# Performance work log

Measured on AMD Instinct MI355X. Metric: run time of the kernel, lower is better.

Reference implementation:

```python
import jax, jax.numpy as jnp
import numpy as np
from jax import lax

DIM = 2048
N_HEADS = 16
N_KV = 4
HEAD_DIM = DIM // N_HEADS  # 128
ROPE_BASE = 10000.0
SEQ = 4096
BSZ = 1


def bitlinear(x, W):
    # per-row abs-mean scale (detached), ternary round/clamp, straight-through blend
    s = lax.stop_gradient(jnp.clip(jnp.mean(jnp.abs(W), axis=1, keepdims=True), 1e-5, None))
    wt = jnp.clip(jnp.round(W / s), -1.0, 1.0)
    w = lax.stop_gradient(wt - W) + W  # straight-through
    return x @ (w * s).T


def rms_norm(x):
    eps = jnp.finfo(x.dtype).eps
    return x * lax.rsqrt(jnp.mean(x * x, axis=-1, keepdims=True) + eps)


def rope(x, cos, sin):
    half = x.shape[-1] // 2
    x1, x2 = x[..., :half], x[..., half:]
    return jnp.concatenate((x1 * cos + x2 * sin, -x1 * sin + x2 * cos), axis=-1)


def setup_inputs() -> dict:
    key = jax.random.key(0)
    ks = jax.random.split(key, 6)
    kv_dim = N_KV * HEAD_DIM
    return {
        "x": jax.random.normal(ks[0], (BSZ, SEQ, DIM), dtype=jnp.float32),
        "wq": jax.random.normal(ks[1], (DIM, DIM), dtype=jnp.float32) * 0.02,
        "wk": jax.random.normal(ks[2], (kv_dim, DIM), dtype=jnp.float32) * 0.02,
        "wv": jax.random.normal(ks[3], (kv_dim, DIM), dtype=jnp.float32) * 0.02,
        "wp": jax.random.normal(ks[4], (DIM, DIM), dtype=jnp.float32) * 0.02,
        "q_gain": jnp.ones((N_HEADS,), dtype=jnp.float32),
    }


def reference(x, wq, wk, wv, wp, q_gain):
    b, s, d = x.shape
    q = bitlinear(x, wq).reshape(b, s, N_HEADS, HEAD_DIM).transpose(0, 2, 1, 3)  # bhsd
    k = bitlinear(x, wk).reshape(b, s, N_KV, HEAD_DIM).transpose(0, 2, 1, 3)
    v = bitlinear(x, wv).reshape(b, s, N_KV, HEAD_DIM).transpose(0, 2, 1, 3)

    q = rms_norm(q)
    k = rms_norm(k)

    inv_freq = 1.0 / ROPE_BASE ** (jnp.arange(0, HEAD_DIM, 2, dtype=jnp.float32) / HEAD_DIM)
    t = jnp.arange(s, dtype=jnp.float32)
    freqs = jnp.outer(t, inv_freq)  # [s, hd/2]
    cos = jnp.cos(freqs)[None, None].astype(q.dtype)
    sin = jnp.sin(freqs)[None, None].astype(q.dtype)
    q = rope(q, cos, sin)
    k = rope(k, cos, sin)

    q = q * q_gain.astype(q.dtype)[None, :, None, None]

    groups = N_HEADS // N_KV
    k = jnp.repeat(k, groups, axis=1)  # GQA expand to [b, H, s, hd]
    v = jnp.repeat(v, groups, axis=1)

    scale = 1.0 / np.sqrt(HEAD_DIM)
    scores = jnp.einsum("bhqd,bhkd->bhqk", q, k) * scale
    causal = jnp.tril(jnp.ones((s, s), dtype=bool))
    scores = jnp.where(causal[None, None], scores, jnp.finfo(scores.dtype).min)
    attn = jax.nn.softmax(scores, axis=-1)
    y = jnp.einsum("bhqk,bhkd->bhqd", attn, v)

    y = y.transpose(0, 2, 1, 3).reshape(b, s, d)
    return bitlinear(y, wp)
```

## Files before the change

### kernel.cpp

```cpp
#include <hip/hip_runtime.h>
#include <math.h>

typedef unsigned short u16;
typedef short s16x8 __attribute__((ext_vector_type(8)));
typedef float f32x4 __attribute__((ext_vector_type(4)));
typedef u16 u16x4 __attribute__((ext_vector_type(4)));

static constexpr size_t OFF_XB   = 0;
static constexpr size_t OFF_WQKV = 16777216;
static constexpr size_t OFF_WP   = 29360128;
static constexpr size_t OFF_QKV  = 37748736;
static constexpr size_t OFF_KH   = 88080384;
static constexpr size_t OFF_VT   = 92274688;

__device__ __forceinline__ u16 f2bf(float f) {
  union { float f; unsigned u; } v; v.f = f;
  unsigned r = v.u + 0x7fffu + ((v.u >> 16) & 1u);
  return (u16)(r >> 16);
}

__device__ __forceinline__ void async16(const u16* g, u16* lds) {
  __builtin_amdgcn_global_load_lds(
      (const __attribute__((address_space(1))) void*)g,
      (__attribute__((address_space(3))) void*)lds, 16, 0, 0);
}

__global__ __launch_bounds__(256) void quant_rows(const float* __restrict__ W,
                                                  u16* __restrict__ out) {
  const int row = blockIdx.x, tid = threadIdx.x;
  const float* src = W + (size_t)row * 2048 + tid * 8;
  float4 a = *(const float4*)(src);
  float4 b = *(const float4*)(src + 4);
  float asum = fabsf(a.x)+fabsf(a.y)+fabsf(a.z)+fabsf(a.w)
             + fabsf(b.x)+fabsf(b.y)+fabsf(b.z)+fabsf(b.w);
  #pragma unroll
  for (int off = 1; off < 64; off <<= 1) asum += __shfl_xor(asum, off, 64);
  __shared__ float red[4];
  if ((tid & 63) == 0) red[tid >> 6] = asum;
  __syncthreads();
  float s = fmaxf((red[0]+red[1]+red[2]+red[3]) * (1.0f/2048.0f), 1e-5f);
  float v[8] = {a.x,a.y,a.z,a.w,b.x,b.y,b.z,b.w};
  u16* dst = out + (size_t)row * 2048 + tid * 8;
  #pragma unroll
  for (int i = 0; i < 8; i++) {
    float q = rintf(v[i] / s);
    q = fminf(fmaxf(q, -1.f), 1.f);
    dst[i] = f2bf(q * s);
  }
}

__global__ __launch_bounds__(256) void cvt_bf16(const float* __restrict__ in,
                                                u16* __restrict__ out) {
  size_t i = ((size_t)blockIdx.x * 256 + threadIdx.x) * 4;
  float4 v = *(const float4*)(in + i);
  u16x4 o;
  o.x = f2bf(v.x); o.y = f2bf(v.y); o.z = f2bf(v.z); o.w = f2bf(v.w);
  *(u16x4*)(out + i) = o;
}

__global__ __launch_bounds__(256) void gemm_bt(const u16* __restrict__ A,
                                               const u16* __restrict__ B,
                                               float* __restrict__ C,
                                               int M, int N, int K) {
  __shared__ u16 sA[128 * 32];
  __shared__ u16 sB[128 * 32];
  const int tid = threadIdx.x;
  const int lane = tid & 63;
  const int wid = tid >> 6;
  const int lr = lane & 15, lq = lane >> 4;
  const int wm = (wid >> 1) * 64, wn = (wid & 1) * 64;
  const size_t m0 = (size_t)blockIdx.y * 128, n0 = (size_t)blockIdx.x * 128;

  const int r0 = tid >> 2, c0 = (tid & 3) * 8;
  const u16* Ab0 = A + (m0 + r0) * (size_t)K + c0;
  const u16* Ab1 = A + (m0 + 64 + r0) * (size_t)K + c0;
  const u16* Bb0 = B + (n0 + r0) * (size_t)K + c0;
  const u16* Bb1 = B + (n0 + 64 + r0) * (size_t)K + c0;
  u16* sA0 = &sA[tid * 8];
  u16* sA1 = &sA[(256 + tid) * 8];
  u16* sB0 = &sB[tid * 8];
  u16* sB1 = &sB[(256 + tid) * 8];

  f32x4 acc[4][4] = {};

  for (int kt = 0; kt < K; kt += 32) {
    async16(Ab0 + kt, sA0);
    async16(Ab1 + kt, sA1);
    async16(Bb0 + kt, sB0);
    async16(Bb1 + kt, sB1);
    __syncthreads();
    s16x8 af[4], bf[4];
    #pragma unroll
    for (int mt = 0; mt < 4; mt++)
      af[mt] = *(const s16x8*)&sA[(wm + mt * 16 + lr) * 32 + lq * 8];
    #pragma unroll
    for (int nt = 0; nt < 4; nt++)
      bf[nt] = *(const s16x8*)&sB[(wn + nt * 16 + lr) * 32 + lq * 8];
    #pragma unroll
    for (int mt = 0; mt < 4; mt++)
      #pragma unroll
      for (int nt = 0; nt < 4; nt++)
        acc[mt][nt] = __builtin_amdgcn_mfma_f32_16x16x32_bf16(af[mt], bf[nt], acc[mt][nt], 0, 0, 0);
    __syncthreads();
  }
  #pragma unroll
  for (int mt = 0; mt < 4; mt++)
    #pragma unroll
    for (int nt = 0; nt < 4; nt++)
      #pragma unroll
      for (int r = 0; r < 4; r++) {
        size_t m = m0 + wm + mt * 16 + lq * 4 + r;
        size_t n = n0 + wn + nt * 16 + lr;
        C[m * (size_t)N + n] = acc[mt][nt][r];
      }
}

__global__ __launch_bounds__(256) void prep_qk(const float* __restrict__ qkv,
                                               const float* __restrict__ qgain,
                                               u16* __restrict__ Qh,
                                               u16* __restrict__ Kh) {
  const int s = blockIdx.y;
  const int j = blockIdx.x * 4 + (threadIdx.x >> 6);
  const int t = threadIdx.x & 63;
  const float* row = qkv + (size_t)s * 3072 + (size_t)j * 128;
  float x1 = row[t], x2 = row[t + 64];
  float ss = x1 * x1 + x2 * x2;
  #pragma unroll
  for (int off = 1; off < 64; off <<= 1) ss += __shfl_xor(ss, off, 64);
  float rn = rsqrtf(ss * (1.0f / 128.0f) + 1.1920929e-07f);
  float invf = exp2f(-(float)t * 0.20762050593048096f);
  float ang = (float)s * invf;
  float sn, c;
  sincosf(ang, &sn, &c);
  if (j < 16) {
    float g = qgain[j] * 0.12751738f;
    float q1 = x1 * rn, q2 = x2 * rn;
    float o1 = (q1 * c + q2 * sn) * g;
    float o2 = (-q1 * sn + q2 * c) * g;
    u16* dst = Qh + ((size_t)j * 4096 + s) * 128;
    dst[t] = f2bf(o1); dst[t + 64] = f2bf(o2);
  } else {
    float k1 = x1 * rn, k2 = x2 * rn;
    float o1 = k1 * c + k2 * sn;
    float o2 = -k1 * sn + k2 * c;
    u16* dst = Kh + ((size_t)(j - 16) * 4096 + s) * 128;
    dst[t] = f2bf(o1); dst[t + 64] = f2bf(o2);
  }
}

__global__ __launch_bounds__(256) void vtrans(const float* __restrict__ qkv,
                                              u16* __restrict__ Vtg) {
  __shared__ float tile[64][67];
  const int tid = threadIdx.x;
  const int s0 = blockIdx.y * 64;
  const int c0 = blockIdx.x * 64;
  #pragma unroll
  for (int it = 0; it < 4; it++) {
    int i = it * 256 + tid;
    int r = i >> 4, c = (i & 15) * 4;
    float4 v = *(const float4*)(qkv + (size_t)(s0 + r) * 3072 + 2560 + c0 + c);
    tile[r][c] = v.x; tile[r][c + 1] = v.y; tile[r][c + 2] = v.z; tile[r][c + 3] = v.w;
  }
  __syncthreads();
  #pragma unroll
  for (int it = 0; it < 2; it++) {
    int i = it * 256 + tid;
    int dl = i >> 3, sc = (i & 7) * 8;
    s16x8 ov;
    #pragma unroll
    for (int jj = 0; jj < 8; jj++) ov[jj] = (short)f2bf(tile[sc + jj][dl]);
    *(s16x8*)&Vtg[(size_t)(c0 + dl) * 4096 + s0 + sc] = ov;
  }
}

__global__ __launch_bounds__(256) void attn(const u16* __restrict__ Q,
                                            const u16* __restrict__ Kh,
                                            const u16* __restrict__ Vt,
                                            u16* __restrict__ Y) {
  const int h = blockIdx.x & 15;
  const int qt = 63 - (blockIdx.x >> 4);
  const int kvh = h >> 2;
  const int tid = threadIdx.x, lane = tid & 63, wid = tid >> 6;
  const int lr = lane & 15, lq = lane >> 4;

  __shared__ u16 sK[64][136];
  __shared__ u16 sVt[128][72];
  __shared__ u16 sP[4][16][72];

  const int q0 = qt * 64;
  s16x8 qf[4];
  {
    const u16* qp = Q + ((size_t)h * 4096 + q0 + wid * 16 + lr) * 128 + lq * 8;
    #pragma unroll
    for (int kc = 0; kc < 4; kc++) qf[kc] = *(const s16x8*)(qp + kc * 32);
  }
  f32x4 oacc[8] = {};
  float mrow[4], lrow[4];
  #pragma unroll
  for (int r = 0; r < 4; r++) { mrow[r] = -1e30f; lrow[r] = 0.f; }

  const u16* Kbase = Kh + (size_t)kvh * 4096 * 128;
  const u16* Vbase = Vt + (size_t)kvh * 128 * 4096;

  for (int t = 0; t <= qt; ++t) {
    #pragma unroll
    for (int it = 0; it < 4; it++) {
      int idx = it * 256 + tid;
      int kr = idx >> 4, kc = (idx & 15) * 8;
      *(s16x8*)&sK[kr][kc] = *(const s16x8*)(Kbase + ((size_t)(t * 64 + kr)) * 128 + kc);
    }
    #pragma unroll
    for (int it = 0; it < 4; it++) {
      int idx = it * 256 + tid;
      int vd = idx >> 3, vc = (idx & 7) * 8;
      *(s16x8*)&sVt[vd][vc] = *(const s16x8*)(Vbase + (size_t)vd * 4096 + t * 64 + vc);
    }
    __syncthreads();

    f32x4 sacc[4] = {};
    #pragma unroll
    for (int nt = 0; nt < 4; nt++)
      #pragma unroll
      for (int kc = 0; kc < 4; kc++) {
        s16x8 kf = *(const s16x8*)&sK[nt * 16 + lr][kc * 32 + lq * 8];
        sacc[nt] = __builtin_amdgcn_mfma_f32_16x16x32_bf16(qf[kc], kf, sacc[nt], 0, 0, 0);
      }
    if (t == qt) {
      #pragma unroll
      for (int nt = 0; nt < 4; nt++)
        #pragma unroll
        for (int r = 0; r < 4; r++)
          if (nt * 16 + lr > wid * 16 + lq * 4 + r) sacc[nt][r] = -1e30f;
    }
    float mx[4];
    #pragma unroll
    for (int r = 0; r < 4; r++)
      mx[r] = fmaxf(fmaxf(sacc[0][r], sacc[1][r]), fmaxf(sacc[2][r], sacc[3][r]));
    #pragma unroll
    for (int off = 1; off < 16; off <<= 1)
      #pragma unroll
      for (int r = 0; r < 4; r++) mx[r] = fmaxf(mx[r], __shfl_xor(mx[r], off, 64));
    float mnew[4], alpha[4], rsum[4];
    #pragma unroll
    for (int r = 0; r < 4; r++) {
      mnew[r] = fmaxf(mrow[r], mx[r]);
      alpha[r] = exp2f(mrow[r] - mnew[r]);
      rsum[r] = 0.f;
    }
    #pragma unroll
    for (int nt = 0; nt < 4; nt++)
      #pragma unroll
      for (int r = 0; r < 4; r++) {
        float p = exp2f(sacc[nt][r] - mnew[r]);
        rsum[r] += p;
        sP[wid][lq * 4 + r][nt * 16 + lr] = f2bf(p);
      }
    #pragma unroll
    for (int off = 1; off < 16; off <<= 1)
      #pragma unroll
      for (int r = 0; r < 4; r++) rsum[r] += __shfl_xor(rsum[r], off, 64);
    #pragma unroll
    for (int r = 0; r < 4; r++) { lrow[r] = lrow[r] * alpha[r] + rsum[r]; mrow[r] = mnew[r]; }
    #pragma unroll
    for (int dt = 0; dt < 8; dt++)
      #pragma unroll
      for (int r = 0; r < 4; r++) oacc[dt][r] *= alpha[r];
    #pragma unroll
    for (int kc = 0; kc < 2; kc++) {
      s16x8 pf = *(const s16x8*)&sP[wid][lr][kc * 32 + lq * 8];
      #pragma unroll
      for (int dt = 0; dt < 8; dt++) {
        s16x8 vf = *(const s16x8*)&sVt[dt * 16 + lr][kc * 32 + lq * 8];
        oacc[dt] = __builtin_amdgcn_mfma_f32_16x16x32_bf16(pf, vf, oacc[dt], 0, 0, 0);
      }
    }
    __syncthreads();
  }
  float invl[4];
  #pragma unroll
  for (int r = 0; r < 4; r++) invl[r] = 1.0f / lrow[r];
  #pragma unroll
  for (int dt = 0; dt < 8; dt++)
    #pragma unroll
    for (int r = 0; r < 4; r++) {
      int qg = q0 + wid * 16 + lq * 4 + r;
      int d = dt * 16 + lr;
      Y[(size_t)qg * 2048 + h * 128 + d] = f2bf(oacc[dt][r] * invl[r]);
    }
}

extern "C" void kernel_launch(void* const* d_in, const int* in_sizes, int n_in,
                              void* d_out, int out_size, void* d_ws, size_t ws_size,
                              hipStream_t stream) {
  const float* x  = (const float*)d_in[0];
  const float* wq = (const float*)d_in[1];
  const float* wk = (const float*)d_in[2];
  const float* wv = (const float*)d_in[3];
  const float* wp = (const float*)d_in[4];
  const float* qg = (const float*)d_in[5];
  float* out = (float*)d_out;
  char* ws = (char*)d_ws;

  u16*   XB   = (u16*)(ws + OFF_XB);
  u16*   WQKV = (u16*)(ws + OFF_WQKV);
  u16*   WP   = (u16*)(ws + OFF_WP);
  float* QKV  = (float*)(ws + OFF_QKV);
  u16*   QH   = XB;
  u16*   KH   = (u16*)(ws + OFF_KH);
  u16*   VT   = (u16*)(ws + OFF_VT);
  u16*   Yb   = (u16*)(ws + OFF_QKV);

  quant_rows<<<2048, 256, 0, stream>>>(wq, WQKV);
  quant_rows<<<512,  256, 0, stream>>>(wk, WQKV + (size_t)2048 * 2048);
  quant_rows<<<512,  256, 0, stream>>>(wv, WQKV + (size_t)2560 * 2048);
  quant_rows<<<2048, 256, 0, stream>>>(wp, WP);
  cvt_bf16<<<8192, 256, 0, stream>>>(x, XB);
  gemm_bt<<<dim3(24, 32), 256, 0, stream>>>(XB, WQKV, QKV, 4096, 3072, 2048);
  prep_qk<<<dim3(5, 4096), 256, 0, stream>>>(QKV, qg, QH, KH);
  vtrans<<<dim3(8, 64), 256, 0, stream>>>(QKV, VT);
  attn<<<1024, 256, 0, stream>>>(QH, KH, VT, Yb);
  gemm_bt<<<dim3(16, 32), 256, 0, stream>>>(Yb, WP, out, 4096, 2048, 2048);
}
```

Baseline: 467.9 us.

## Use 128-row query tiles with split-KV for long tiles and combine kernel

The attention kernel now processes 128 query rows per block, with each wave handling two 16-row fragments, so every K/V tile loaded into LDS is reused twice as much. Query tiles in the upper half of the sequence are split into two KV chunks whose partial outputs and max/sum statistics go to a workspace, and a new combine kernel merges them. Blocks are ordered longest-first for load balance. Other changes: the row sum is taken from a ones-row appended to V via MFMA, the accumulator rescale is skipped when no row max grows, and the launch bounds request two blocks per CU. The cost is more registers per thread, an extra kernel launch, extra workspace traffic, and bf16 truncation instead of rounding for P.

```diff
diff --git a/kernel.cpp b/kernel.cpp
--- a/kernel.cpp
+++ b/kernel.cpp
@@ -10,6 +10,7 @@
 static constexpr size_t OFF_WQKV = 16777216;
 static constexpr size_t OFF_WP   = 29360128;
 static constexpr size_t OFF_QKV  = 37748736;
+static constexpr size_t OFF_PART = 37748736 + 16777216;
 static constexpr size_t OFF_KH   = 88080384;
 static constexpr size_t OFF_VT   = 92274688;
 
@@ -173,41 +174,62 @@
   }
 }
 
-__global__ __launch_bounds__(256) void attn(const u16* __restrict__ Q,
-                                            const u16* __restrict__ Kh,
-                                            const u16* __restrict__ Vt,
-                                            u16* __restrict__ Y) {
-  const int h = blockIdx.x & 15;
-  const int qt = 63 - (blockIdx.x >> 4);
-  const int kvh = h >> 2;
+__global__ __launch_bounds__(256, 2) void attn(const u16* __restrict__ Q,
+                                               const u16* __restrict__ Kh,
+                                               const u16* __restrict__ Vt,
+                                               u16* __restrict__ Y,
+                                               float* __restrict__ Opart,
+                                               float* __restrict__ MLpart) {
   const int tid = threadIdx.x, lane = tid & 63, wid = tid >> 6;
   const int lr = lane & 15, lq = lane >> 4;
 
+  int rem = blockIdx.x, s = 32;
+  for (;;) {
+    int cnt = (s >= 17 ? 32 : 0) + (((s & 1) == 0) ? 16 : 0);
+    if (rem < cnt) break;
+    rem -= cnt; --s;
+  }
+  int qt, chunk, h, split;
+  if (s >= 17 && rem < 32) { split = 1; qt = s - 1; chunk = rem >> 4; h = rem & 15; }
+  else { split = 0; if (s >= 17) rem -= 32; qt = (s >> 1) - 1; chunk = 0; h = rem & 15; }
+  const int t0 = split ? chunk * (qt + 1) : 0;
+  const int t1 = split ? t0 + qt + 1 : 2 * qt + 2;
+  const int kvh = h >> 2;
+  const int qbase = qt * 128;
+
   __shared__ u16 sK[64][136];
-  __shared__ u16 sVt[128][72];
-  __shared__ u16 sP[4][16][72];
-
-  const int q0 = qt * 64;
-  s16x8 qf[4];
-  {
-    const u16* qp = Q + ((size_t)h * 4096 + q0 + wid * 16 + lr) * 128 + lq * 8;
-    #pragma unroll
-    for (int kc = 0; kc < 4; kc++) qf[kc] = *(const s16x8*)(qp + kc * 32);
-  }
-  f32x4 oacc[8] = {};
-  float mrow[4], lrow[4];
-  #pragma unroll
-  for (int r = 0; r < 4; r++) { mrow[r] = -1e30f; lrow[r] = 0.f; }
+  __shared__ u16 sVt[144][72];
+  __shared__ u16 sP[4][32][72];
+
+  for (int i = tid; i < 16 * 72; i += 256) {
+    int r = i / 72, c = i - r * 72;
+    sVt[128 + r][c] = (r == 0) ? (u16)0x3F80 : (u16)0;
+  }
+
+  s16x8 qf[2][4];
+  #pragma unroll
+  for (int f = 0; f < 2; f++) {
+    const u16* qp = Q + ((size_t)h * 4096 + qbase + wid * 32 + f * 16 + lr) * 128 + lq * 8;
+    #pragma unroll
+    for (int kc = 0; kc < 4; kc++) qf[f][kc] = *(const s16x8*)(qp + kc * 32);
+  }
+
+  f32x4 oacc[2][9] = {};
+  float mrow[2][4];
+  #pragma unroll
+  for (int f = 0; f < 2; f++)
+    #pragma unroll
+    for (int r = 0; r < 4; r++) mrow[f][r] = -1e30f;
 
   const u16* Kbase = Kh + (size_t)kvh * 4096 * 128;
   const u16* Vbase = Vt + (size_t)kvh * 128 * 4096;
 
-  for (int t = 0; t <= qt; ++t) {
+  for (int t = t0; t < t1; ++t) {
     #pragma unroll
     for (int it = 0; it < 4; it++) {
       int idx = it * 256 + tid;
-      int kr = idx >> 4, kc = (idx & 15) * 8;
-      *(s16x8*)&sK[kr][kc] = *(const s16x8*)(Kbase + ((size_t)(t * 64 + kr)) * 128 + kc);
+      int kr = idx >> 4, kc8 = (idx & 15) * 8;
+      *(s16x8*)&sK[kr][kc8] = *(const s16x8*)(Kbase + (size_t)(t * 64 + kr) * 128 + kc8);
     }
     #pragma unroll
     for (int it = 0; it < 4; it++) {
@@ -217,76 +239,165 @@
     }
     __syncthreads();
 
-    f32x4 sacc[4] = {};
+    f32x4 sacc[2][4] = {};
     #pragma unroll
     for (int nt = 0; nt < 4; nt++)
       #pragma unroll
       for (int kc = 0; kc < 4; kc++) {
         s16x8 kf = *(const s16x8*)&sK[nt * 16 + lr][kc * 32 + lq * 8];
-        sacc[nt] = __builtin_amdgcn_mfma_f32_16x16x32_bf16(qf[kc], kf, sacc[nt], 0, 0, 0);
+        sacc[0][nt] = __builtin_amdgcn_mfma_f32_16x16x32_bf16(qf[0][kc], kf, sacc[0][nt], 0, 0, 0);
+        sacc[1][nt] = __builtin_amdgcn_mfma_f32_16x16x32_bf16(qf[1][kc], kf, sacc[1][nt], 0, 0, 0);
       }
-    if (t == qt) {
+
+    if (t >= 2 * qt) {
+      #pragma unroll
+      for (int f = 0; f < 2; f++) {
+        int qr0 = qbase + wid * 32 + f * 16 + lq * 4;
+        #pragma unroll
+        for (int nt = 0; nt < 4; nt++) {
+          int col = t * 64 + nt * 16 + lr;
+          #pragma unroll
+          for (int r = 0; r < 4; r++)
+            if (col > qr0 + r) sacc[f][nt][r] = -1e30f;
+        }
+      }
+    }
+
+    float mx[2][4];
+    #pragma unroll
+    for (int f = 0; f < 2; f++)
+      #pragma unroll
+      for (int r = 0; r < 4; r++)
+        mx[f][r] = fmaxf(fmaxf(sacc[f][0][r], sacc[f][1][r]),
+                         fmaxf(sacc[f][2][r], sacc[f][3][r]));
+    #pragma unroll
+    for (int off = 1; off < 16; off <<= 1)
+      #pragma unroll
+      for (int f = 0; f < 2; f++)
+        #pragma unroll
+        for (int r = 0; r < 4; r++) mx[f][r] = fmaxf(mx[f][r], __shfl_xor(mx[f][r], off, 64));
+
+    bool grow = false;
+    #pragma unroll
+    for (int f = 0; f < 2; f++)
+      #pragma unroll
+      for (int r = 0; r < 4; r++) grow = grow || (mx[f][r] > mrow[f][r]);
+    if (__any(grow)) {
+      float al[2][4];
+      #pragma unroll
+      for (int f = 0; f < 2; f++)
+        #pragma unroll
+        for (int r = 0; r < 4; r++) {
+          float mn = fmaxf(mrow[f][r], mx[f][r]);
+          al[f][r] = exp2f(mrow[f][r] - mn);
+          mrow[f][r] = mn;
+        }
+      #pragma unroll
+      for (int f = 0; f < 2; f++)
+        #pragma unroll
+        for (int dt = 0; dt < 9; dt++)
+          #pragma unroll
+          for (int r = 0; r < 4; r++) oacc[f][dt][r] *= al[f][r];
+    }
+
+    #pragma unroll
+    for (int f = 0; f < 2; f++)
       #pragma unroll
       for (int nt = 0; nt < 4; nt++)
         #pragma unroll
+        for (int r = 0; r < 4; r++) {
+          union { float fv; unsigned u; } pu;
+          pu.fv = exp2f(sacc[f][nt][r] - mrow[f][r]);
+          sP[wid][f * 16 + lq * 4 + r][nt * 16 + lr] = (u16)(pu.u >> 16);
+        }
+
+    #pragma unroll
+    for (int kc = 0; kc < 2; kc++) {
+      s16x8 pf0 = *(const s16x8*)&sP[wid][lr][kc * 32 + lq * 8];
+      s16x8 pf1 = *(const s16x8*)&sP[wid][16 + lr][kc * 32 + lq * 8];
+      #pragma unroll
+      for (int dt = 0; dt < 9; dt++) {
+        s16x8 vf = *(const s16x8*)&sVt[dt * 16 + lr][kc * 32 + lq * 8];
+        oacc[0][dt] = __builtin_amdgcn_mfma_f32_16x16x32_bf16(pf0, vf, oacc[0][dt], 0, 0, 0);
+        oacc[1][dt] = __builtin_amdgcn_mfma_f32_16x16x32_bf16(pf1, vf, oacc[1][dt], 0, 0, 0);
+      }
+    }
+    __syncthreads();
+  }
+
+  if (split) {
+    const int pidx = ((qt - 16) * 16 + h) * 2 + chunk;
+    float* Op = Opart + (size_t)pidx * 16384;
+    #pragma unroll
+    for (int f = 0; f < 2; f++)
+      #pragma unroll
+      for (int dt = 0; dt < 8; dt++)
+        #pragma unroll
         for (int r = 0; r < 4; r++)
-          if (nt * 16 + lr > wid * 16 + lq * 4 + r) sacc[nt][r] = -1e30f;
-    }
-    float mx[4];
-    #pragma unroll
-    for (int r = 0; r < 4; r++)
-      mx[r] = fmaxf(fmaxf(sacc[0][r], sacc[1][r]), fmaxf(sacc[2][r], sacc[3][r]));
-    #pragma unroll
-    for (int off = 1; off < 16; off <<= 1)
-      #pragma unroll
-      for (int r = 0; r < 4; r++) mx[r] = fmaxf(mx[r], __shfl_xor(mx[r], off, 64));
-    float mnew[4], alpha[4], rsum[4];
-    #pragma unroll
-    for (int r = 0; r < 4; r++) {
-      mnew[r] = fmaxf(mrow[r], mx[r]);
-      alpha[r] = exp2f(mrow[r] - mnew[r]);
-      rsum[r] = 0.f;
-    }
-    #pragma unroll
-    for (int nt = 0; nt < 4; nt++)
+          Op[(wid * 32 + f * 16 + lq * 4 + r) * 128 + dt * 16 + lr] = oacc[f][dt][r];
+    if (lr == 0) {
+      #pragma unroll
+      for (int f = 0; f < 2; f++)
+        #pragma unroll
+        for (int r = 0; r < 4; r++) {
+          int row = wid * 32 + f * 16 + lq * 4 + r;
+          MLpart[(size_t)pidx * 256 + row * 2]     = mrow[f][r];
+          MLpart[(size_t)pidx * 256 + row * 2 + 1] = oacc[f][8][r];
+        }
+    }
+  } else {
+    #pragma unroll
+    for (int f = 0; f < 2; f++) {
+      float linv[4];
       #pragma unroll
       for (int r = 0; r < 4; r++) {
-        float p = exp2f(sacc[nt][r] - mnew[r]);
-        rsum[r] += p;
-        sP[wid][lq * 4 + r][nt * 16 + lr] = f2bf(p);
+        float lv = __shfl(oacc[f][8][r], lane & 48);
+        linv[r] = 1.0f / lv;
       }
-    #pragma unroll
-    for (int off = 1; off < 16; off <<= 1)
-      #pragma unroll
-      for (int r = 0; r < 4; r++) rsum[r] += __shfl_xor(rsum[r], off, 64);
-    #pragma unroll
-    for (int r = 0; r < 4; r++) { lrow[r] = lrow[r] * alpha[r] + rsum[r]; mrow[r] = mnew[r]; }
-    #pragma unroll
-    for (int dt = 0; dt < 8; dt++)
-      #pragma unroll
-      for (int r = 0; r < 4; r++) oacc[dt][r] *= alpha[r];
-    #pragma unroll
-    for (int kc = 0; kc < 2; kc++) {
-      s16x8 pf = *(const s16x8*)&sP[wid][lr][kc * 32 + lq * 8];
-      #pragma unroll
-      for (int dt = 0; dt < 8; dt++) {
-        s16x8 vf = *(const s16x8*)&sVt[dt * 16 + lr][kc * 32 + lq * 8];
-        oacc[dt] = __builtin_amdgcn_mfma_f32_16x16x32_bf16(pf, vf, oacc[dt], 0, 0, 0);
-      }
-    }
-    __syncthreads();
-  }
-  float invl[4];
-  #pragma unroll
-  for (int r = 0; r < 4; r++) invl[r] = 1.0f / lrow[r];
-  #pragma unroll
-  for (int dt = 0; dt < 8; dt++)
-    #pragma unroll
-    for (int r = 0; r < 4; r++) {
-      int qg = q0 + wid * 16 + lq * 4 + r;
-      int d = dt * 16 + lr;
-      Y[(size_t)qg * 2048 + h * 128 + d] = f2bf(oacc[dt][r] * invl[r]);
-    }
+      #pragma unroll
+      for (int dt = 0; dt < 8; dt++)
+        #pragma unroll
+        for (int r = 0; r < 4; r++) {
+          int q = qbase + wid * 32 + f * 16 + lq * 4 + r;
+          Y[(size_t)q * 2048 + h * 128 + dt * 16 + lr] = f2bf(oacc[f][dt][r] * linv[r]);
+        }
+    }
+  }
+}
+
+__global__ __launch_bounds__(256) void combine(const float* __restrict__ Op,
+                                               const float* __restrict__ ML,
+                                               u16* __restrict__ Y) {
+  const int blk = blockIdx.x;
+  const int qt16 = blk >> 4, h = blk & 15;
+  const int p0 = blk * 2, p1 = p0 + 1;
+  const int tid = threadIdx.x;
+  const int row = tid >> 1, half = (tid & 1) * 64;
+  float m0 = ML[(size_t)p0 * 256 + row * 2], l0 = ML[(size_t)p0 * 256 + row * 2 + 1];
+  float m1 = ML[(size_t)p1 * 256 + row * 2], l1 = ML[(size_t)p1 * 256 + row * 2 + 1];
+  float m = fmaxf(m0, m1);
+  float w0 = exp2f(m0 - m), w1 = exp2f(m1 - m);
+  float inv = 1.0f / (l0 * w0 + l1 * w1);
+  w0 *= inv; w1 *= inv;
+  const float* o0 = Op + (size_t)p0 * 16384 + row * 128 + half;
+  const float* o1 = Op + (size_t)p1 * 16384 + row * 128 + half;
+  size_t q = (size_t)(qt16 + 16) * 128 + row;
+  u16* dst = Y + q * 2048 + h * 128 + half;
+  #pragma unroll
+  for (int c = 0; c < 64; c += 8) {
+    float4 a0 = *(const float4*)(o0 + c), b0 = *(const float4*)(o0 + c + 4);
+    float4 a1 = *(const float4*)(o1 + c), b1 = *(const float4*)(o1 + c + 4);
+    u16 tmp[8];
+    tmp[0] = f2bf(a0.x * w0 + a1.x * w1);
+    tmp[1] = f2bf(a0.y * w0 + a1.y * w1);
+    tmp[2] = f2bf(a0.z * w0 + a1.z * w1);
+    tmp[3] = f2bf(a0.w * w0 + a1.w * w1);
+    tmp[4] = f2bf(b0.x * w0 + b1.x * w1);
+    tmp[5] = f2bf(b0.y * w0 + b1.y * w1);
+    tmp[6] = f2bf(b0.z * w0 + b1.z * w1);
+    tmp[7] = f2bf(b0.w * w0 + b1.w * w1);
+    *(s16x8*)(dst + c) = *(s16x8*)tmp;
+  }
 }
 
 extern "C" void kernel_launch(void* const* d_in, const int* in_sizes, int n_in,
@@ -301,14 +412,16 @@
   float* out = (float*)d_out;
   char* ws = (char*)d_ws;
 
-  u16*   XB   = (u16*)(ws + OFF_XB);
-  u16*   WQKV = (u16*)(ws + OFF_WQKV);
-  u16*   WP   = (u16*)(ws + OFF_WP);
-  float* QKV  = (float*)(ws + OFF_QKV);
-  u16*   QH   = XB;
-  u16*   KH   = (u16*)(ws + OFF_KH);
-  u16*   VT   = (u16*)(ws + OFF_VT);
-  u16*   Yb   = (u16*)(ws + OFF_QKV);
+  u16*   XB    = (u16*)(ws + OFF_XB);
+  u16*   WQKV  = (u16*)(ws + OFF_WQKV);
+  u16*   WP    = (u16*)(ws + OFF_WP);
+  float* QKV   = (float*)(ws + OFF_QKV);
+  u16*   QH    = XB;
+  u16*   KH    = (u16*)(ws + OFF_KH);
+  u16*   VT    = (u16*)(ws + OFF_VT);
+  u16*   Yb    = (u16*)(ws + OFF_QKV);
+  float* OPART = (float*)(ws + OFF_PART);
+  float* MLP   = (float*)(ws + OFF_WQKV);
 
   quant_rows<<<2048, 256, 0, stream>>>(wq, WQKV);
   quant_rows<<<512,  256, 0, stream>>>(wk, WQKV + (size_t)2048 * 2048);
@@ -318,6 +431,7 @@
   gemm_bt<<<dim3(24, 32), 256, 0, stream>>>(XB, WQKV, QKV, 4096, 3072, 2048);
   prep_qk<<<dim3(5, 4096), 256, 0, stream>>>(QKV, qg, QH, KH);
   vtrans<<<dim3(8, 64), 256, 0, stream>>>(QKV, VT);
-  attn<<<1024, 256, 0, stream>>>(QH, KH, VT, Yb);
+  attn<<<768, 256, 0, stream>>>(QH, KH, VT, Yb, OPART, MLP);
+  combine<<<256, 256, 0, stream>>>(OPART, MLP, Yb);
   gemm_bt<<<dim3(16, 32), 256, 0, stream>>>(Yb, WP, out, 4096, 2048, 2048);
 }
```

New measurement: 438.2 us. 6.3% less time.
